# Performance work log

Hardware: AMD Instinct MI355X
Metric: run time of the kernel (lower is better)

The kernel has to match this reference:

```python
import jax, jax.numpy as jnp
import numpy as np

EPS = 1e-12  # F.normalize eps


def setup_inputs() -> dict:
    key = jax.random.key(0)
    k1, k2 = jax.random.split(key)
    B, T, C, E = 4, 4096, 2048, 64
    return {
        "hidden_states": jax.random.normal(k1, (B, T, C), dtype=jnp.float32),
        "sim_matrix": jax.random.normal(k2, (C, E), dtype=jnp.float32),
        "gates": jnp.zeros((E,), dtype=jnp.float32),
        "min_experts": 2,
    }


def reference(hidden_states, sim_matrix, gates, min_experts):
    b, t, c = hidden_states.shape
    h = hidden_states.reshape(b * t, c)
    # L2-normalize tokens (dim=-1) and expert columns (dim=0)
    hn = h / jnp.maximum(jnp.linalg.norm(h, axis=-1, keepdims=True), EPS)
    wn = sim_matrix / jnp.maximum(jnp.linalg.norm(sim_matrix, axis=0, keepdims=True), EPS)
    logits = hn @ wn - jax.nn.sigmoid(gates)          # [N, E]
    gated = jax.nn.relu(logits)
    # STE threshold (forward: hard 0/1 indicator)
    ind = (gated > 0).astype(gated.dtype)
    mask = gated + jax.lax.stop_gradient(ind - gated)
    # fallback: rows with no active expert get top-min_experts of raw logits
    inactive = jnp.sum(ind, axis=1) == 0              # [N]
    _, topk_idx = jax.lax.top_k(logits, min_experts)  # [N, k]
    n = mask.shape[0]
    fallback = jnp.zeros((n, logits.shape[1]), dtype=bool).at[
        jnp.arange(n)[:, None], topk_idx].set(True)
    put = inactive[:, None] & fallback                # positions overwritten with 1.0
    mask = jnp.where(put, jnp.asarray(1.0, mask.dtype), mask)
    masked = jnp.where(mask > 0, gated, -jnp.inf)
    routing_weights = jax.nn.softmax(masked, axis=-1)
    return routing_weights, logits, mask
```

## Files before the change

### kernel.cpp

```cpp
#include <hip/hip_runtime.h>
#include <math.h>

#define CDIM 2048
#define EDIM 64
#define BM   32
#define NIT  32
#define PREPB 32

#define SCALE_H 1024.0f
#define SCALE_W 4096.0f
#define INV_SCALE (1.0f / 4194304.0f)

typedef float    f32x16 __attribute__((ext_vector_type(16)));
typedef float    f32x4v __attribute__((ext_vector_type(4)));
typedef _Float16 f16x8  __attribute__((ext_vector_type(8)));
typedef __fp16   cvt_t  __attribute__((ext_vector_type(2)));

__global__ void prep_w(const float* __restrict__ W,
                       unsigned short* __restrict__ bfrag,
                       float* __restrict__ pnw) {
    __shared__ float tile[64][65];
    __shared__ float part[4][64];
    const int t = threadIdx.x;
    const int c0 = blockIdx.x * 64;
#pragma unroll
    for (int p = 0; p < 4; ++p) {
        int r = (t >> 4) + p * 16;
        float4 v = *reinterpret_cast<const float4*>(W + (size_t)(c0 + r) * EDIM + (t & 15) * 4);
        tile[r][(t & 15) * 4 + 0] = v.x;
        tile[r][(t & 15) * 4 + 1] = v.y;
        tile[r][(t & 15) * 4 + 2] = v.z;
        tile[r][(t & 15) * 4 + 3] = v.w;
    }
    __syncthreads();
    {
        int g = t >> 6, e = t & 63;
        float s = 0.f;
#pragma unroll
        for (int j = 0; j < 16; ++j) { float v = tile[g * 16 + j][e]; s += v * v; }
        part[g][e] = s;
    }
    __syncthreads();
    if (t < 64) pnw[blockIdx.x * EDIM + t] = part[0][t] + part[1][t] + part[2][t] + part[3][t];
    const int nt = t >> 7, hl = (t >> 6) & 1, lane = t & 63;
    const int e = nt * 32 + (lane & 31);
    const int kb = (lane >> 5) * 8;
#pragma unroll
    for (int s = 0; s < 4; ++s) {
        int kl = s * 16 + kb;
        unsigned int wds[4];
#pragma unroll
        for (int pj = 0; pj < 4; ++pj) {
            float v0 = tile[kl + 2 * pj][e] * SCALE_W;
            float v1 = tile[kl + 2 * pj + 1][e] * SCALE_W;
            cvt_t hh = __builtin_amdgcn_cvt_pkrtz(v0, v1);
            if (hl) {
                cvt_t ll = __builtin_amdgcn_cvt_pkrtz(v0 - (float)hh[0], v1 - (float)hh[1]);
                wds[pj] = __builtin_bit_cast(unsigned int, ll);
            } else {
                wds[pj] = __builtin_bit_cast(unsigned int, hh);
            }
        }
        size_t off = ((size_t)(blockIdx.x * 4 + s)) * 2048 + (size_t)nt * 1024 + (size_t)hl * 512 + (size_t)lane * 8;
        *reinterpret_cast<uint4*>(bfrag + off) = make_uint4(wds[0], wds[1], wds[2], wds[3]);
    }
}

template<int BUF>
__device__ __forceinline__ void stage_it(
    int it, int e, int ks, int w, int l, int row0,
    const float* __restrict__ H, const unsigned short* __restrict__ bfrag,
    float (&aS)[2][2][32][32], unsigned short (&bS)[4][2][4][512])
{
    if (e == 0) {
#pragma unroll
        for (int J = 0; J < 4; ++J) {
            const float* srcA = H + (size_t)(row0 + 8 * J + (l >> 3)) * CDIM
                              + ks * 1024 + it * 32 + (((l & 7) ^ (l >> 3)) << 2);
            __builtin_amdgcn_global_load_lds(
                (const __attribute__((address_space(1))) unsigned int*)srcA,
                (__attribute__((address_space(3))) unsigned int*)&aS[ks][BUF][8 * J][0], 16, 0, 0);
        }
    }
#pragma unroll
    for (int m = 0; m < 4; ++m) {
        const unsigned short* srcB = bfrag + (size_t)(ks * 64 + it * 2 + (m >> 1)) * 2048
                                   + (size_t)e * 1024 + (size_t)(m & 1) * 512 + (size_t)l * 8;
        __builtin_amdgcn_global_load_lds(
            (const __attribute__((address_space(1))) unsigned int*)srcB,
            (__attribute__((address_space(3))) unsigned int*)&bS[w][BUF][m][0], 16, 0, 0);
    }
}

template<int CUR, int STG>
__device__ __forceinline__ void kstep(
    int it, int e, int ks, int w, int l, int row0,
    const float* __restrict__ H, const unsigned short* __restrict__ bfrag,
    float (&aS)[2][2][32][32], unsigned short (&bS)[4][2][4][512],
    f32x16* acc, float& nacc)
{
    if (STG) stage_it<CUR ^ 1>(it + 1, e, ks, w, l, row0, H, bfrag, aS, bS);
    if (STG) {
        if (e == 0) { asm volatile("s_waitcnt vmcnt(8)" ::: "memory"); }
        else        { asm volatile("s_waitcnt vmcnt(4)" ::: "memory"); }
    } else {
        asm volatile("s_waitcnt vmcnt(0)" ::: "memory");
    }
    __builtin_amdgcn_sched_barrier(0);
    __builtin_amdgcn_s_barrier();
    __builtin_amdgcn_sched_barrier(0);

    const int r = l & 31, kg = l >> 5;
#pragma unroll
    for (int j = 0; j < 2; ++j) {
        const f32x4v a0 = *reinterpret_cast<const f32x4v*>(
            &aS[ks][CUR][r][((4 * j + 2 * kg + 0) ^ (r & 7)) * 4]);
        const f32x4v a1 = *reinterpret_cast<const f32x4v*>(
            &aS[ks][CUR][r][((4 * j + 2 * kg + 1) ^ (r & 7)) * 4]);
        float f0 = a0[0], f1 = a0[1], f2 = a0[2], f3 = a0[3];
        float f4 = a1[0], f5 = a1[1], f6 = a1[2], f7 = a1[3];
        nacc += f0*f0 + f1*f1 + f2*f2 + f3*f3 + f4*f4 + f5*f5 + f6*f6 + f7*f7;
        float s0 = f0*SCALE_H, s1 = f1*SCALE_H, s2 = f2*SCALE_H, s3 = f3*SCALE_H;
        float s4 = f4*SCALE_H, s5 = f5*SCALE_H, s6 = f6*SCALE_H, s7 = f7*SCALE_H;
        cvt_t h0 = __builtin_amdgcn_cvt_pkrtz(s0, s1);
        cvt_t h1 = __builtin_amdgcn_cvt_pkrtz(s2, s3);
        cvt_t h2 = __builtin_amdgcn_cvt_pkrtz(s4, s5);
        cvt_t h3 = __builtin_amdgcn_cvt_pkrtz(s6, s7);
        cvt_t l0 = __builtin_amdgcn_cvt_pkrtz(s0 - (float)h0[0], s1 - (float)h0[1]);
        cvt_t l1 = __builtin_amdgcn_cvt_pkrtz(s2 - (float)h1[0], s3 - (float)h1[1]);
        cvt_t l2 = __builtin_amdgcn_cvt_pkrtz(s4 - (float)h2[0], s5 - (float)h2[1]);
        cvt_t l3 = __builtin_amdgcn_cvt_pkrtz(s6 - (float)h3[0], s7 - (float)h3[1]);
        f16x8 ah = __builtin_bit_cast(f16x8, make_uint4(
            __builtin_bit_cast(unsigned int, h0), __builtin_bit_cast(unsigned int, h1),
            __builtin_bit_cast(unsigned int, h2), __builtin_bit_cast(unsigned int, h3)));
        f16x8 al = __builtin_bit_cast(f16x8, make_uint4(
            __builtin_bit_cast(unsigned int, l0), __builtin_bit_cast(unsigned int, l1),
            __builtin_bit_cast(unsigned int, l2), __builtin_bit_cast(unsigned int, l3)));
        f16x8 bh = *reinterpret_cast<const f16x8*>(&bS[w][CUR][2 * j + 0][l * 8]);
        f16x8 bl = *reinterpret_cast<const f16x8*>(&bS[w][CUR][2 * j + 1][l * 8]);
        acc[0] = __builtin_amdgcn_mfma_f32_32x32x16_f16(ah, bh, acc[0], 0, 0, 0);
        acc[1] = __builtin_amdgcn_mfma_f32_32x32x16_f16(ah, bl, acc[1], 0, 0, 0);
        acc[2] = __builtin_amdgcn_mfma_f32_32x32x16_f16(al, bh, acc[2], 0, 0, 0);
    }
    __builtin_amdgcn_sched_barrier(0);
    __builtin_amdgcn_s_barrier();
    __builtin_amdgcn_sched_barrier(0);
}

__launch_bounds__(256, 2)
__global__ void gating_main(const float* __restrict__ H,
                            const unsigned short* __restrict__ bfrag,
                            const float* __restrict__ pnw,
                            const float* __restrict__ gates,
                            float* __restrict__ out_rw,
                            float* __restrict__ out_lg,
                            float* __restrict__ out_mk) {
    __shared__ float aS[2][2][32][32];
    __shared__ unsigned short bS[4][2][4][512];
    __shared__ float red[2][32][36];
    __shared__ float normred[2][32];
    __shared__ float invw_s[64];
    __shared__ float sig_s[64];

    const int t = threadIdx.x;
    const int w = t >> 6, l = t & 63;
    const int e = w & 1, ks = w >> 1;
    const int row0 = blockIdx.x * BM;
    const int kg = l >> 5, arow = l & 31;

    if (t < 64) {
        float s2 = 0.f;
#pragma unroll
        for (int b = 0; b < PREPB; ++b) s2 += pnw[b * EDIM + t];
        invw_s[t] = 1.f / fmaxf(sqrtf(s2), 1e-12f);
        sig_s[t] = 1.f / (1.f + __expf(-gates[t]));
    }
    __builtin_amdgcn_sched_barrier(0);

    f32x16 acc[3];
#pragma unroll
    for (int b = 0; b < 3; ++b)
#pragma unroll
        for (int i = 0; i < 16; ++i) acc[b][i] = 0.f;
    float nacc = 0.f;

    stage_it<0>(0, e, ks, w, l, row0, H, bfrag, aS, bS);
    for (int ot = 0; ot < 15; ++ot) {
        kstep<0, 1>(2 * ot,     e, ks, w, l, row0, H, bfrag, aS, bS, acc, nacc);
        kstep<1, 1>(2 * ot + 1, e, ks, w, l, row0, H, bfrag, aS, bS, acc, nacc);
    }
    kstep<0, 1>(30, e, ks, w, l, row0, H, bfrag, aS, bS, acc, nacc);
    kstep<1, 0>(31, e, ks, w, l, row0, H, bfrag, aS, bS, acc, nacc);

    nacc += __shfl_xor(nacc, 32);
    if (e == 0 && l < 32) normred[ks][l] = nacc;
    if (ks == 0) {
#pragma unroll
        for (int r = 0; r < 16; ++r) {
            int rowl = (r & 3) + 8 * (r >> 2) + 4 * kg;
            red[e][rowl][arow] = acc[0][r] + acc[1][r] + acc[2][r];
        }
    }
    __syncthreads();
    if (ks == 1) {
#pragma unroll
        for (int r = 0; r < 16; ++r) {
            int rowl = (r & 3) + 8 * (r >> 2) + 4 * kg;
            red[e][rowl][arow] += acc[0][r] + acc[1][r] + acc[2][r];
        }
    }
    __syncthreads();

    const int rr = t >> 3, e0 = (t & 7) * 8;
    const int orow = row0 + rr;
    const int eh = e0 >> 5, ec = e0 & 31;
    float nh = normred[0][rr] + normred[1][rr];
    float invh = INV_SCALE / fmaxf(sqrtf(nh), 1e-12f);
    float lg[8];
#pragma unroll
    for (int k2 = 0; k2 < 8; ++k2) {
        int ee = e0 + k2;
        lg[k2] = red[eh][rr][ec + k2] * invh * invw_s[ee] - sig_s[ee];
    }
    float* plg = out_lg + (size_t)orow * EDIM + e0;
    *reinterpret_cast<float4*>(plg)     = make_float4(lg[0], lg[1], lg[2], lg[3]);
    *reinterpret_cast<float4*>(plg + 4) = make_float4(lg[4], lg[5], lg[6], lg[7]);

    float v1 = -INFINITY, v2 = -INFINITY;
    int i1 = 0x7fffffff, i2 = 0x7fffffff, cnt = 0;
#pragma unroll
    for (int j = 0; j < 8; ++j) {
        int ee = e0 + j;
        float v = lg[j];
        cnt += (v > 0.f) ? 1 : 0;
        if (v > v1) { v2 = v1; i2 = i1; v1 = v; i1 = ee; }
        else if (v > v2) { v2 = v; i2 = ee; }
    }
#pragma unroll
    for (int st = 1; st <= 4; st <<= 1) {
        float w1 = __shfl_xor(v1, st);
        int   j1 = __shfl_xor(i1, st);
        float wv2 = __shfl_xor(v2, st);
        int   j2 = __shfl_xor(i2, st);
        int   cc = __shfl_xor(cnt, st);
        cnt += cc;
        bool g = (w1 > v1) || (w1 == v1 && j1 < i1);
        if (g) {
            bool g2 = (v1 > wv2) || (v1 == wv2 && i1 < j2);
            float nv2 = g2 ? v1 : wv2;
            int   ni2 = g2 ? i1 : j2;
            v1 = w1; i1 = j1; v2 = nv2; i2 = ni2;
        } else {
            bool g2 = (w1 > v2) || (w1 == v2 && j1 < i2);
            if (g2) { v2 = w1; i2 = j1; }
        }
    }
    bool act = cnt > 0;
    float rmax = act ? v1 : 0.f;
    float xs[8], ms[8];
    float wsum = 0.f;
#pragma unroll
    for (int j = 0; j < 8; ++j) {
        int ee = e0 + j;
        float lv = lg[j];
        float x, m;
        if (act) {
            bool sel = lv > 0.f;
            m = sel ? 1.f : 0.f;
            x = sel ? __expf(lv - rmax) : 0.f;
        } else {
            bool sel = (ee == i1) || (ee == i2);
            m = sel ? 1.f : 0.f;
            x = m;
        }
        xs[j] = x; ms[j] = m; wsum += x;
    }
    wsum += __shfl_xor(wsum, 1);
    wsum += __shfl_xor(wsum, 2);
    wsum += __shfl_xor(wsum, 4);
    float invd = 1.f / wsum;
    float* prw = out_rw + (size_t)orow * EDIM + e0;
    float* pmk = out_mk + (size_t)orow * EDIM + e0;
    *reinterpret_cast<float4*>(prw)     = make_float4(xs[0]*invd, xs[1]*invd, xs[2]*invd, xs[3]*invd);
    *reinterpret_cast<float4*>(prw + 4) = make_float4(xs[4]*invd, xs[5]*invd, xs[6]*invd, xs[7]*invd);
    *reinterpret_cast<float4*>(pmk)     = make_float4(ms[0], ms[1], ms[2], ms[3]);
    *reinterpret_cast<float4*>(pmk + 4) = make_float4(ms[4], ms[5], ms[6], ms[7]);
}

extern "C" void kernel_launch(void* const* d_in, const int* in_sizes, int n_in,
                              void* d_out, int out_size, void* d_ws, size_t ws_size,
                              hipStream_t stream) {
    const float* H     = (const float*)d_in[0];
    const float* Wm    = (const float*)d_in[1];
    const float* gates = (const float*)d_in[2];
    const int ntok = in_sizes[0] / CDIM;

    unsigned short* bfrag = (unsigned short*)d_ws;
    float* pnw = (float*)(bfrag + (size_t)128 * 2048);

    float* out_rw = (float*)d_out;
    float* out_lg = out_rw + (size_t)ntok * EDIM;
    float* out_mk = out_lg + (size_t)ntok * EDIM;

    hipLaunchKernelGGL(prep_w, dim3(PREPB), dim3(256), 0, stream, Wm, bfrag, pnw);
    hipLaunchKernelGGL(gating_main, dim3(ntok / BM), dim3(256), 0, stream,
                       H, bfrag, pnw, gates, out_rw, out_lg, out_mk);
}
```

Baseline: 40.81 us.

## Deepen A-tile prefetch to four LDS buffers with three-ahead staging

```diff
diff --git a/kernel.cpp b/kernel.cpp
--- a/kernel.cpp
+++ b/kernel.cpp
@@ -67,24 +67,28 @@
 }
 
 template<int BUF>
-__device__ __forceinline__ void stage_it(
-    int it, int e, int ks, int w, int l, int row0,
-    const float* __restrict__ H, const unsigned short* __restrict__ bfrag,
-    float (&aS)[2][2][32][32], unsigned short (&bS)[4][2][4][512])
+__device__ __forceinline__ void stage_A(
+    int itA, int ks, int l, int row0,
+    const float* __restrict__ H, float (&aS)[2][4][32][32])
 {
-    if (e == 0) {
-#pragma unroll
-        for (int J = 0; J < 4; ++J) {
-            const float* srcA = H + (size_t)(row0 + 8 * J + (l >> 3)) * CDIM
-                              + ks * 1024 + it * 32 + (((l & 7) ^ (l >> 3)) << 2);
-            __builtin_amdgcn_global_load_lds(
-                (const __attribute__((address_space(1))) unsigned int*)srcA,
-                (__attribute__((address_space(3))) unsigned int*)&aS[ks][BUF][8 * J][0], 16, 0, 0);
-        }
-    }
+#pragma unroll
+    for (int J = 0; J < 4; ++J) {
+        const float* srcA = H + (size_t)(row0 + 8 * J + (l >> 3)) * CDIM
+                          + ks * 1024 + itA * 32 + (((l & 7) ^ (l >> 3)) << 2);
+        __builtin_amdgcn_global_load_lds(
+            (const __attribute__((address_space(1))) unsigned int*)srcA,
+            (__attribute__((address_space(3))) unsigned int*)&aS[ks][BUF][8 * J][0], 16, 0, 0);
+    }
+}
+
+template<int BUF>
+__device__ __forceinline__ void stage_B(
+    int itB, int e, int ks, int w, int l,
+    const unsigned short* __restrict__ bfrag, unsigned short (&bS)[4][2][4][512])
+{
 #pragma unroll
     for (int m = 0; m < 4; ++m) {
-        const unsigned short* srcB = bfrag + (size_t)(ks * 64 + it * 2 + (m >> 1)) * 2048
+        const unsigned short* srcB = bfrag + (size_t)(ks * 64 + itB * 2 + (m >> 1)) * 2048
                                    + (size_t)e * 1024 + (size_t)(m & 1) * 512 + (size_t)l * 8;
         __builtin_amdgcn_global_load_lds(
             (const __attribute__((address_space(1))) unsigned int*)srcB,
@@ -92,20 +96,22 @@
     }
 }
 
-template<int CUR, int STG>
+template<int CURA, int CURB, bool FIRST>
 __device__ __forceinline__ void kstep(
     int it, int e, int ks, int w, int l, int row0,
     const float* __restrict__ H, const unsigned short* __restrict__ bfrag,
-    float (&aS)[2][2][32][32], unsigned short (&bS)[4][2][4][512],
+    float (&aS)[2][4][32][32], unsigned short (&bS)[4][2][4][512],
     f32x16* acc, float& nacc)
 {
-    if (STG) stage_it<CUR ^ 1>(it + 1, e, ks, w, l, row0, H, bfrag, aS, bS);
-    if (STG) {
-        if (e == 0) { asm volatile("s_waitcnt vmcnt(8)" ::: "memory"); }
-        else        { asm volatile("s_waitcnt vmcnt(4)" ::: "memory"); }
-    } else {
-        asm volatile("s_waitcnt vmcnt(0)" ::: "memory");
-    }
+    const int itB = (it + 1 < NIT) ? it + 1 : NIT - 1;
+    const int itA = (it + 3 < NIT) ? it + 3 : NIT - 1;
+    stage_B<CURB ^ 1>(itB, e, ks, w, l, bfrag, bS);
+    if (e == 0) stage_A<(CURA + 3) & 3>(itA, ks, l, row0, H, aS);
+
+    if (e == 0) {
+        if (FIRST) { asm volatile("s_waitcnt vmcnt(16)" ::: "memory"); }
+        else       { asm volatile("s_waitcnt vmcnt(12)" ::: "memory"); }
+    } else       {   asm volatile("s_waitcnt vmcnt(4)"  ::: "memory"); }
     __builtin_amdgcn_sched_barrier(0);
     __builtin_amdgcn_s_barrier();
     __builtin_amdgcn_sched_barrier(0);
@@ -114,9 +120,9 @@
 #pragma unroll
     for (int j = 0; j < 2; ++j) {
         const f32x4v a0 = *reinterpret_cast<const f32x4v*>(
-            &aS[ks][CUR][r][((4 * j + 2 * kg + 0) ^ (r & 7)) * 4]);
+            &aS[ks][CURA][r][((4 * j + 2 * kg + 0) ^ (r & 7)) * 4]);
         const f32x4v a1 = *reinterpret_cast<const f32x4v*>(
-            &aS[ks][CUR][r][((4 * j + 2 * kg + 1) ^ (r & 7)) * 4]);
+            &aS[ks][CURA][r][((4 * j + 2 * kg + 1) ^ (r & 7)) * 4]);
         float f0 = a0[0], f1 = a0[1], f2 = a0[2], f3 = a0[3];
         float f4 = a1[0], f5 = a1[1], f6 = a1[2], f7 = a1[3];
         nacc += f0*f0 + f1*f1 + f2*f2 + f3*f3 + f4*f4 + f5*f5 + f6*f6 + f7*f7;
@@ -136,8 +142,8 @@
         f16x8 al = __builtin_bit_cast(f16x8, make_uint4(
             __builtin_bit_cast(unsigned int, l0), __builtin_bit_cast(unsigned int, l1),
             __builtin_bit_cast(unsigned int, l2), __builtin_bit_cast(unsigned int, l3)));
-        f16x8 bh = *reinterpret_cast<const f16x8*>(&bS[w][CUR][2 * j + 0][l * 8]);
-        f16x8 bl = *reinterpret_cast<const f16x8*>(&bS[w][CUR][2 * j + 1][l * 8]);
+        f16x8 bh = *reinterpret_cast<const f16x8*>(&bS[w][CURB][2 * j + 0][l * 8]);
+        f16x8 bl = *reinterpret_cast<const f16x8*>(&bS[w][CURB][2 * j + 1][l * 8]);
         acc[0] = __builtin_amdgcn_mfma_f32_32x32x16_f16(ah, bh, acc[0], 0, 0, 0);
         acc[1] = __builtin_amdgcn_mfma_f32_32x32x16_f16(ah, bl, acc[1], 0, 0, 0);
         acc[2] = __builtin_amdgcn_mfma_f32_32x32x16_f16(al, bh, acc[2], 0, 0, 0);
@@ -155,7 +161,7 @@
                             float* __restrict__ out_rw,
                             float* __restrict__ out_lg,
                             float* __restrict__ out_mk) {
-    __shared__ float aS[2][2][32][32];
+    __shared__ float aS[2][4][32][32];
     __shared__ unsigned short bS[4][2][4][512];
     __shared__ float red[2][32][36];
     __shared__ float normred[2][32];
@@ -184,13 +190,24 @@
         for (int i = 0; i < 16; ++i) acc[b][i] = 0.f;
     float nacc = 0.f;
 
-    stage_it<0>(0, e, ks, w, l, row0, H, bfrag, aS, bS);
-    for (int ot = 0; ot < 15; ++ot) {
-        kstep<0, 1>(2 * ot,     e, ks, w, l, row0, H, bfrag, aS, bS, acc, nacc);
-        kstep<1, 1>(2 * ot + 1, e, ks, w, l, row0, H, bfrag, aS, bS, acc, nacc);
-    }
-    kstep<0, 1>(30, e, ks, w, l, row0, H, bfrag, aS, bS, acc, nacc);
-    kstep<1, 0>(31, e, ks, w, l, row0, H, bfrag, aS, bS, acc, nacc);
+    stage_B<0>(0, e, ks, w, l, bfrag, bS);
+    if (e == 0) {
+        stage_A<0>(0, ks, l, row0, H, aS);
+        stage_A<1>(1, ks, l, row0, H, aS);
+        stage_A<2>(2, ks, l, row0, H, aS);
+    }
+
+    kstep<0, 0, true >(0, e, ks, w, l, row0, H, bfrag, aS, bS, acc, nacc);
+    kstep<1, 1, false>(1, e, ks, w, l, row0, H, bfrag, aS, bS, acc, nacc);
+    kstep<2, 0, false>(2, e, ks, w, l, row0, H, bfrag, aS, bS, acc, nacc);
+    kstep<3, 1, false>(3, e, ks, w, l, row0, H, bfrag, aS, bS, acc, nacc);
+    for (int ot = 1; ot < 8; ++ot) {
+        kstep<0, 0, false>(4 * ot,     e, ks, w, l, row0, H, bfrag, aS, bS, acc, nacc);
+        kstep<1, 1, false>(4 * ot + 1, e, ks, w, l, row0, H, bfrag, aS, bS, acc, nacc);
+        kstep<2, 0, false>(4 * ot + 2, e, ks, w, l, row0, H, bfrag, aS, bS, acc, nacc);
+        kstep<3, 1, false>(4 * ot + 3, e, ks, w, l, row0, H, bfrag, aS, bS, acc, nacc);
+    }
+    asm volatile("s_waitcnt vmcnt(0)" ::: "memory");
 
     nacc += __shfl_xor(nacc, 32);
     if (e == 0 && l < 32) normred[ks][l] = nacc;
```

New measurement: 42.97 us. 5.3% more time.

## Split K across four waves with private A staging and register-loaded B

Applied to the files above, without the earlier changes.

```diff
diff --git a/kernel.cpp b/kernel.cpp
--- a/kernel.cpp
+++ b/kernel.cpp
@@ -4,7 +4,7 @@
 #define CDIM 2048
 #define EDIM 64
 #define BM   32
-#define NIT  32
+#define NITW 16
 #define PREPB 32
 
 #define SCALE_H 1024.0f
@@ -12,7 +12,7 @@
 #define INV_SCALE (1.0f / 4194304.0f)
 
 typedef float    f32x16 __attribute__((ext_vector_type(16)));
-typedef float    f32x4v __attribute__((ext_vector_type(4)));
+typedef float    f32x4  __attribute__((ext_vector_type(4)));
 typedef _Float16 f16x8  __attribute__((ext_vector_type(8)));
 typedef __fp16   cvt_t  __attribute__((ext_vector_type(2)));
 
@@ -67,56 +67,50 @@
 }
 
 template<int BUF>
-__device__ __forceinline__ void stage_it(
-    int it, int e, int ks, int w, int l, int row0,
+__device__ __forceinline__ void stageA(int it, int w, int l, int row0,
+    const float* __restrict__ H, float (&aS)[4][2][32][32]) {
+#pragma unroll
+    for (int J = 0; J < 4; ++J) {
+        const int row_ = 8 * J + (l >> 3);
+        const float* src = H + (size_t)(row0 + row_) * CDIM + w * 512 + it * 32
+                         + (((l & 7) ^ (row_ & 7)) << 2);
+        __builtin_amdgcn_global_load_lds(
+            (const __attribute__((address_space(1))) unsigned int*)src,
+            (__attribute__((address_space(3))) unsigned int*)&aS[w][BUF][8 * J][0], 16, 0, 0);
+    }
+}
+
+__device__ __forceinline__ void loadB(int it, int w, int l,
+    const unsigned short* __restrict__ bfrag, uint4 (&b)[8]) {
+    const int kc0 = w * 32 + it * 2;
+#pragma unroll
+    for (int kc2 = 0; kc2 < 2; ++kc2)
+#pragma unroll
+        for (int nt = 0; nt < 2; ++nt)
+#pragma unroll
+            for (int hl = 0; hl < 2; ++hl)
+                b[kc2 * 4 + nt * 2 + hl] = *reinterpret_cast<const uint4*>(
+                    bfrag + (size_t)(kc0 + kc2) * 2048 + nt * 1024 + hl * 512 + (size_t)l * 8);
+}
+
+template<int BUF, bool LAST>
+__device__ __forceinline__ void kstep(int it, int w, int l, int row0,
     const float* __restrict__ H, const unsigned short* __restrict__ bfrag,
-    float (&aS)[2][2][32][32], unsigned short (&bS)[4][2][4][512])
-{
-    if (e == 0) {
-#pragma unroll
-        for (int J = 0; J < 4; ++J) {
-            const float* srcA = H + (size_t)(row0 + 8 * J + (l >> 3)) * CDIM
-                              + ks * 1024 + it * 32 + (((l & 7) ^ (l >> 3)) << 2);
-            __builtin_amdgcn_global_load_lds(
-                (const __attribute__((address_space(1))) unsigned int*)srcA,
-                (__attribute__((address_space(3))) unsigned int*)&aS[ks][BUF][8 * J][0], 16, 0, 0);
-        }
-    }
-#pragma unroll
-    for (int m = 0; m < 4; ++m) {
-        const unsigned short* srcB = bfrag + (size_t)(ks * 64 + it * 2 + (m >> 1)) * 2048
-                                   + (size_t)e * 1024 + (size_t)(m & 1) * 512 + (size_t)l * 8;
-        __builtin_amdgcn_global_load_lds(
-            (const __attribute__((address_space(1))) unsigned int*)srcB,
-            (__attribute__((address_space(3))) unsigned int*)&bS[w][BUF][m][0], 16, 0, 0);
-    }
-}
-
-template<int CUR, int STG>
-__device__ __forceinline__ void kstep(
-    int it, int e, int ks, int w, int l, int row0,
-    const float* __restrict__ H, const unsigned short* __restrict__ bfrag,
-    float (&aS)[2][2][32][32], unsigned short (&bS)[4][2][4][512],
-    f32x16* acc, float& nacc)
-{
-    if (STG) stage_it<CUR ^ 1>(it + 1, e, ks, w, l, row0, H, bfrag, aS, bS);
-    if (STG) {
-        if (e == 0) { asm volatile("s_waitcnt vmcnt(8)" ::: "memory"); }
-        else        { asm volatile("s_waitcnt vmcnt(4)" ::: "memory"); }
-    } else {
-        asm volatile("s_waitcnt vmcnt(0)" ::: "memory");
-    }
+    float (&aS)[4][2][32][32], f32x16 (&acc)[2], float& nacc) {
+    uint4 bcur[8];
+    loadB(it, w, l, bfrag, bcur);
+    if (!LAST) stageA<BUF ^ 1>(it + 1, w, l, row0, H, aS);
     __builtin_amdgcn_sched_barrier(0);
-    __builtin_amdgcn_s_barrier();
+    if (LAST) { asm volatile("s_waitcnt vmcnt(0)" ::: "memory"); }
+    else      { asm volatile("s_waitcnt vmcnt(4)" ::: "memory"); }
     __builtin_amdgcn_sched_barrier(0);
 
     const int r = l & 31, kg = l >> 5;
 #pragma unroll
-    for (int j = 0; j < 2; ++j) {
-        const f32x4v a0 = *reinterpret_cast<const f32x4v*>(
-            &aS[ks][CUR][r][((4 * j + 2 * kg + 0) ^ (r & 7)) * 4]);
-        const f32x4v a1 = *reinterpret_cast<const f32x4v*>(
-            &aS[ks][CUR][r][((4 * j + 2 * kg + 1) ^ (r & 7)) * 4]);
+    for (int kc2 = 0; kc2 < 2; ++kc2) {
+        const int c0 = kc2 * 4 + kg * 2;
+        f32x4 a0 = *reinterpret_cast<const f32x4*>(&aS[w][BUF][r][((c0)     ^ (r & 7)) * 4]);
+        f32x4 a1 = *reinterpret_cast<const f32x4*>(&aS[w][BUF][r][((c0 + 1) ^ (r & 7)) * 4]);
         float f0 = a0[0], f1 = a0[1], f2 = a0[2], f3 = a0[3];
         float f4 = a1[0], f5 = a1[1], f6 = a1[2], f7 = a1[3];
         nacc += f0*f0 + f1*f1 + f2*f2 + f3*f3 + f4*f4 + f5*f5 + f6*f6 + f7*f7;
@@ -136,18 +130,20 @@
         f16x8 al = __builtin_bit_cast(f16x8, make_uint4(
             __builtin_bit_cast(unsigned int, l0), __builtin_bit_cast(unsigned int, l1),
             __builtin_bit_cast(unsigned int, l2), __builtin_bit_cast(unsigned int, l3)));
-        f16x8 bh = *reinterpret_cast<const f16x8*>(&bS[w][CUR][2 * j + 0][l * 8]);
-        f16x8 bl = *reinterpret_cast<const f16x8*>(&bS[w][CUR][2 * j + 1][l * 8]);
-        acc[0] = __builtin_amdgcn_mfma_f32_32x32x16_f16(ah, bh, acc[0], 0, 0, 0);
-        acc[1] = __builtin_amdgcn_mfma_f32_32x32x16_f16(ah, bl, acc[1], 0, 0, 0);
-        acc[2] = __builtin_amdgcn_mfma_f32_32x32x16_f16(al, bh, acc[2], 0, 0, 0);
-    }
-    __builtin_amdgcn_sched_barrier(0);
-    __builtin_amdgcn_s_barrier();
-    __builtin_amdgcn_sched_barrier(0);
-}
-
-__launch_bounds__(256, 2)
+        f16x8 bh0 = __builtin_bit_cast(f16x8, bcur[kc2 * 4 + 0]);
+        f16x8 bl0 = __builtin_bit_cast(f16x8, bcur[kc2 * 4 + 1]);
+        f16x8 bh1 = __builtin_bit_cast(f16x8, bcur[kc2 * 4 + 2]);
+        f16x8 bl1 = __builtin_bit_cast(f16x8, bcur[kc2 * 4 + 3]);
+        acc[0] = __builtin_amdgcn_mfma_f32_32x32x16_f16(ah, bh0, acc[0], 0, 0, 0);
+        acc[1] = __builtin_amdgcn_mfma_f32_32x32x16_f16(ah, bh1, acc[1], 0, 0, 0);
+        acc[0] = __builtin_amdgcn_mfma_f32_32x32x16_f16(ah, bl0, acc[0], 0, 0, 0);
+        acc[1] = __builtin_amdgcn_mfma_f32_32x32x16_f16(ah, bl1, acc[1], 0, 0, 0);
+        acc[0] = __builtin_amdgcn_mfma_f32_32x32x16_f16(al, bh0, acc[0], 0, 0, 0);
+        acc[1] = __builtin_amdgcn_mfma_f32_32x32x16_f16(al, bh1, acc[1], 0, 0, 0);
+    }
+}
+
+__launch_bounds__(256, 3)
 __global__ void gating_main(const float* __restrict__ H,
                             const unsigned short* __restrict__ bfrag,
                             const float* __restrict__ pnw,
@@ -155,19 +151,43 @@
                             float* __restrict__ out_rw,
                             float* __restrict__ out_lg,
                             float* __restrict__ out_mk) {
-    __shared__ float aS[2][2][32][32];
-    __shared__ unsigned short bS[4][2][4][512];
-    __shared__ float red[2][32][36];
-    __shared__ float normred[2][32];
-    __shared__ float invw_s[64];
-    __shared__ float sig_s[64];
+    __shared__ float aS[4][2][32][32];
+    __shared__ float normred[4][32];
+    __shared__ float invw_s[64], sig_s[64];
 
     const int t = threadIdx.x;
     const int w = t >> 6, l = t & 63;
-    const int e = w & 1, ks = w >> 1;
     const int row0 = blockIdx.x * BM;
     const int kg = l >> 5, arow = l & 31;
 
+    f32x16 acc[2];
+#pragma unroll
+    for (int a = 0; a < 2; ++a)
+#pragma unroll
+        for (int i = 0; i < 16; ++i) acc[a][i] = 0.f;
+    float nacc = 0.f;
+
+    stageA<0>(0, w, l, row0, H, aS);
+#pragma unroll
+    for (int ot = 0; ot < 7; ++ot) {
+        kstep<0, false>(2 * ot,     w, l, row0, H, bfrag, aS, acc, nacc);
+        kstep<1, false>(2 * ot + 1, w, l, row0, H, bfrag, aS, acc, nacc);
+    }
+    kstep<0, false>(14, w, l, row0, H, bfrag, aS, acc, nacc);
+    kstep<1, true >(15, w, l, row0, H, bfrag, aS, acc, nacc);
+
+    __syncthreads();
+
+    float* redp = &aS[0][0][0][0];
+#pragma unroll
+    for (int nt = 0; nt < 2; ++nt)
+#pragma unroll
+        for (int r = 0; r < 16; ++r) {
+            int row = (r & 3) + 8 * (r >> 2) + 4 * kg;
+            redp[((size_t)w * 32 + row) * 64 + nt * 32 + arow] = acc[nt][r];
+        }
+    nacc += __shfl_xor(nacc, 32);
+    if (l < 32) normred[w][l] = nacc;
     if (t < 64) {
         float s2 = 0.f;
 #pragma unroll
@@ -175,52 +195,19 @@
         invw_s[t] = 1.f / fmaxf(sqrtf(s2), 1e-12f);
         sig_s[t] = 1.f / (1.f + __expf(-gates[t]));
     }
-    __builtin_amdgcn_sched_barrier(0);
-
-    f32x16 acc[3];
-#pragma unroll
-    for (int b = 0; b < 3; ++b)
-#pragma unroll
-        for (int i = 0; i < 16; ++i) acc[b][i] = 0.f;
-    float nacc = 0.f;
-
-    stage_it<0>(0, e, ks, w, l, row0, H, bfrag, aS, bS);
-    for (int ot = 0; ot < 15; ++ot) {
-        kstep<0, 1>(2 * ot,     e, ks, w, l, row0, H, bfrag, aS, bS, acc, nacc);
-        kstep<1, 1>(2 * ot + 1, e, ks, w, l, row0, H, bfrag, aS, bS, acc, nacc);
-    }
-    kstep<0, 1>(30, e, ks, w, l, row0, H, bfrag, aS, bS, acc, nacc);
-    kstep<1, 0>(31, e, ks, w, l, row0, H, bfrag, aS, bS, acc, nacc);
-
-    nacc += __shfl_xor(nacc, 32);
-    if (e == 0 && l < 32) normred[ks][l] = nacc;
-    if (ks == 0) {
-#pragma unroll
-        for (int r = 0; r < 16; ++r) {
-            int rowl = (r & 3) + 8 * (r >> 2) + 4 * kg;
-            red[e][rowl][arow] = acc[0][r] + acc[1][r] + acc[2][r];
-        }
-    }
-    __syncthreads();
-    if (ks == 1) {
-#pragma unroll
-        for (int r = 0; r < 16; ++r) {
-            int rowl = (r & 3) + 8 * (r >> 2) + 4 * kg;
-            red[e][rowl][arow] += acc[0][r] + acc[1][r] + acc[2][r];
-        }
-    }
     __syncthreads();
 
     const int rr = t >> 3, e0 = (t & 7) * 8;
     const int orow = row0 + rr;
-    const int eh = e0 >> 5, ec = e0 & 31;
-    float nh = normred[0][rr] + normred[1][rr];
+    float nh = normred[0][rr] + normred[1][rr] + normred[2][rr] + normred[3][rr];
     float invh = INV_SCALE / fmaxf(sqrtf(nh), 1e-12f);
     float lg[8];
 #pragma unroll
     for (int k2 = 0; k2 < 8; ++k2) {
         int ee = e0 + k2;
-        lg[k2] = red[eh][rr][ec + k2] * invh * invw_s[ee] - sig_s[ee];
+        float s = redp[(0 * 32 + rr) * 64 + ee] + redp[(1 * 32 + rr) * 64 + ee]
+                + redp[(2 * 32 + rr) * 64 + ee] + redp[(3 * 32 + rr) * 64 + ee];
+        lg[k2] = s * invh * invw_s[ee] - sig_s[ee];
     }
     float* plg = out_lg + (size_t)orow * EDIM + e0;
     *reinterpret_cast<float4*>(plg)     = make_float4(lg[0], lg[1], lg[2], lg[3]);
@@ -296,7 +283,7 @@
     const int ntok = in_sizes[0] / CDIM;
 
     unsigned short* bfrag = (unsigned short*)d_ws;
-    float* pnw = (float*)(bfrag + (size_t)128 * 2048);
+    float* pnw = (float*)(bfrag + (size_t)262144);
 
     float* out_rw = (float*)d_out;
     float* out_lg = out_rw + (size_t)ntok * EDIM;
```

After: 36.06 us, median of 2. 1.13x faster.
